# Kernel optimization log

Hardware: AMD Instinct MI355X
Metric: run time of the kernel (lower is better)

The kernel has to match this reference:

```python
import jax, jax.numpy as jnp
import numpy as np

N = 50000
E = 800000
IN_DIM = 128
HIDDEN = 32
HEADS = 4
OUT_DIM = 64
NEG_SLOPE = 0.2


def _glorot(key, shape):
    fan_in, fan_out = shape[0], shape[-1]
    lim = jnp.sqrt(6.0 / (fan_in + fan_out))
    return jax.random.uniform(key, shape, jnp.float32, -lim, lim)


def setup_inputs() -> dict:
    key = jax.random.key(0)
    ks = jax.random.split(key, 16)
    x = jax.random.normal(ks[0], (N, IN_DIM), jnp.float32)
    edge_index = jax.random.randint(ks[1], (2, E), 0, N, jnp.int64)
    # layer 0: in_dim -> hidden, heads, concat
    W1 = _glorot(ks[2], (IN_DIM, HEADS * HIDDEN))
    a_src1 = _glorot(ks[3], (HEADS, HIDDEN))
    a_dst1 = _glorot(ks[4], (HEADS, HIDDEN))
    b1 = jnp.zeros((HEADS * HIDDEN,), jnp.float32)
    # layer 1: hidden*heads -> hidden, heads, concat
    W2 = _glorot(ks[5], (HEADS * HIDDEN, HEADS * HIDDEN))
    a_src2 = _glorot(ks[6], (HEADS, HIDDEN))
    a_dst2 = _glorot(ks[7], (HEADS, HIDDEN))
    b2 = jnp.zeros((HEADS * HIDDEN,), jnp.float32)
    # layer 2: hidden*heads -> out_dim, heads, concat=False (mean over heads)
    W3 = _glorot(ks[8], (HEADS * HIDDEN, HEADS * OUT_DIM))
    a_src3 = _glorot(ks[9], (HEADS, OUT_DIM))
    a_dst3 = _glorot(ks[10], (HEADS, OUT_DIM))
    b3 = jnp.zeros((OUT_DIM,), jnp.float32)
    return {"x": x, "edge_index": edge_index,
            "W1": W1, "a_src1": a_src1, "a_dst1": a_dst1, "b1": b1,
            "W2": W2, "a_src2": a_src2, "a_dst2": a_dst2, "b2": b2,
            "W3": W3, "a_src3": a_src3, "a_dst3": a_dst3, "b3": b3}


def gat_conv(x, src, dst, W, a_src, a_dst, bias, out_ch, concat):
    # linear projection, per-head view: [N, H, C]
    h = (x @ W).reshape(N, HEADS, out_ch)
    # per-node attention logits, gathered to edges: [E, H]
    alpha_src = jnp.einsum('nhc,hc->nh', h, a_src)
    alpha_dst = jnp.einsum('nhc,hc->nh', h, a_dst)
    e = jax.nn.leaky_relu(alpha_src[src] + alpha_dst[dst], NEG_SLOPE)
    # segment softmax over incoming edges of each dst node
    m = jax.ops.segment_max(e, dst, num_segments=N)  # [N, H]
    m = jnp.where(jnp.isfinite(m), m, 0.0)
    p = jnp.exp(e - m[dst])  # [E, H]
    denom = jax.ops.segment_sum(p, dst, num_segments=N)  # [N, H]
    alpha = p / (denom[dst] + 1e-16)
    # weighted scatter-add of source features: [N, H, C]
    out = jax.ops.segment_sum(h[src] * alpha[:, :, None], dst, num_segments=N)
    if concat:
        return out.reshape(N, HEADS * out_ch) + bias
    return out.mean(axis=1) + bias


def reference(x, edge_index, W1, a_src1, a_dst1, b1, W2, a_src2, a_dst2, b2,
              W3, a_src3, a_dst3, b3):
    src, dst = edge_index[0], edge_index[1]
    x = gat_conv(x, src, dst, W1, a_src1, a_dst1, b1, HIDDEN, True)
    x = gat_conv(x, src, dst, W2, a_src2, a_dst2, b2, HIDDEN, True)
    x = gat_conv(x, src, dst, W3, a_src3, a_dst3, b3, OUT_DIM, False)
    return x
```

## Files before the change

kernel.cpp:

```cpp
#include <hip/hip_runtime.h>
#include <hip/hip_fp16.h>
#include <math.h>

#define NNODES 50000
#define NEDGES 800000

typedef _Float16 half8 __attribute__((ext_vector_type(8)));
typedef float floatx4 __attribute__((ext_vector_type(4)));


__global__ void zero_i32(int* __restrict__ p, int n) {
    int i = blockIdx.x * 256 + threadIdx.x;
    if (i < n) p[i] = 0;
}

__global__ void hist_kernel(const int* __restrict__ dst, int* __restrict__ counts, int e) {
    int i = blockIdx.x * 256 + threadIdx.x;
    if (i < e) atomicAdd(&counts[dst[i]], 1);
}

__global__ void scan1_kernel(const int* __restrict__ counts, int* __restrict__ row_ptr,
                             int* __restrict__ bsums, int n) {
    __shared__ int s[256];
    int tid = threadIdx.x;
    int i = blockIdx.x * 256 + tid;
    int v = (i < n) ? counts[i] : 0;
    s[tid] = v;
    __syncthreads();
    #pragma unroll
    for (int o = 1; o < 256; o <<= 1) {
        int t = (tid >= o) ? s[tid - o] : 0;
        __syncthreads();
        s[tid] += t;
        __syncthreads();
    }
    if (i < n) row_ptr[i + 1] = s[tid];
    if (tid == 255) bsums[blockIdx.x] = s[255];
}

__global__ void scan2_kernel(int* __restrict__ bsums, int nb) {
    __shared__ int s[256];
    int tid = threadIdx.x;
    int v = (tid < nb) ? bsums[tid] : 0;
    s[tid] = v;
    __syncthreads();
    #pragma unroll
    for (int o = 1; o < 256; o <<= 1) {
        int t = (tid >= o) ? s[tid - o] : 0;
        __syncthreads();
        s[tid] += t;
        __syncthreads();
    }
    if (tid < nb) bsums[tid] = s[tid] - v;
}

__global__ void scan3_kernel(int* __restrict__ row_ptr, const int* __restrict__ bsums,
                             int* __restrict__ cursor, int n) {
    int i = blockIdx.x * 256 + threadIdx.x;
    if (i < n) {
        row_ptr[i + 1] += bsums[blockIdx.x];
        cursor[i] = 0;
    }
    if (i == 0) row_ptr[0] = 0;
}

__global__ void fill_kernel(const int* __restrict__ src, const int* __restrict__ dst,
                            const int* __restrict__ row_ptr, int* __restrict__ cursor,
                            int* __restrict__ csr_src, int e) {
    int i = blockIdx.x * 256 + threadIdx.x;
    if (i < e) {
        int d = dst[i];
        int pos = atomicAdd(&cursor[d], 1);
        csr_src[row_ptr[d] + pos] = src[i];
    }
}

__global__ void prep_v_kernel(const float* __restrict__ W3, const float* __restrict__ as3,
                              const float* __restrict__ ad3, float* __restrict__ Vs,
                              float* __restrict__ Vd) {
    int id = blockIdx.x * 256 + threadIdx.x;
    if (id >= 1024) return;
    int which = id >> 9;
    int rem = id & 511;
    int k = rem >> 2;
    int hd = rem & 3;
    const float* av = which ? ad3 : as3;
    float s = 0.f;
    #pragma unroll 8
    for (int c = 0; c < 64; ++c)
        s += W3[(size_t)k * 256 + hd * 64 + c] * av[hd * 64 + c];
    (which ? Vd : Vs)[hd * 128 + k] = s;
}

__global__ void prep_wr_kernel(const float* __restrict__ W3, __half* __restrict__ Wr) {
    int id = blockIdx.x * 256 + threadIdx.x;
    if (id >= 64 * 512) return;
    int c = id >> 9;
    int rem = id & 511;
    int hd = rem >> 7;
    int k = rem & 127;
    Wr[(size_t)c * 512 + hd * 128 + k] = __float2half(W3[(size_t)k * 256 + hd * 64 + c]);
}


template <bool AF32, int LAYER>
__global__ __launch_bounds__(256, 3) void gemm_mfma(const void* __restrict__ A_,
                                                    const float* __restrict__ Wf,
                                                    const float* __restrict__ a_src,
                                                    const float* __restrict__ a_dst,
                                                    __half* __restrict__ H,
                                                    float* __restrict__ asrc,
                                                    float* __restrict__ adst, int n) {
    const int M = 128, CH = 32;
    __shared__ __half As[128][136];
    __shared__ __half Ws[64][136];
    int tid = threadIdx.x;
    int row0 = blockIdx.x * 128;
    int col0 = blockIdx.y * 64;

    if constexpr (AF32) {
        const float* Af = (const float*)A_;
        #pragma unroll
        for (int it = 0; it < 8; ++it) {
            int flat = tid + it * 256;
            int r = flat >> 4;
            int kq = (flat & 15) * 8;
            int gr = row0 + r;
            float4 v0 = {0.f, 0.f, 0.f, 0.f}, v1 = {0.f, 0.f, 0.f, 0.f};
            if (gr < n) {
                v0 = *(const float4*)&Af[(size_t)gr * 128 + kq];
                v1 = *(const float4*)&Af[(size_t)gr * 128 + kq + 4];
            }
            __half2 h0 = __floats2half2_rn(v0.x, v0.y);
            __half2 h1 = __floats2half2_rn(v0.z, v0.w);
            __half2 h2 = __floats2half2_rn(v1.x, v1.y);
            __half2 h3 = __floats2half2_rn(v1.z, v1.w);
            uint4 st = {*(unsigned*)&h0, *(unsigned*)&h1, *(unsigned*)&h2, *(unsigned*)&h3};
            *(uint4*)&As[r][kq] = st;
        }
    } else {
        const __half* Ah = (const __half*)A_;
        #pragma unroll
        for (int it = 0; it < 8; ++it) {
            int flat = tid + it * 256;
            int r = flat >> 4;
            int kq = (flat & 15) * 8;
            int gr = row0 + r;
            float4 v = {0.f, 0.f, 0.f, 0.f};
            if (gr < n) v = *(const float4*)&Ah[(size_t)gr * 128 + kq];
            *(float4*)&As[r][kq] = v;
        }
    }
    #pragma unroll
    for (int it = 0; it < 4; ++it) {
        int flat = tid + it * 256;
        int kp = flat >> 4;
        int c4 = (flat & 15) * 4;
        int k = kp * 2;
        float4 va = *(const float4*)&Wf[(size_t)k * M + col0 + c4];
        float4 vb = *(const float4*)&Wf[(size_t)(k + 1) * M + col0 + c4];
        *(__half2*)&Ws[c4 + 0][k] = __floats2half2_rn(va.x, vb.x);
        *(__half2*)&Ws[c4 + 1][k] = __floats2half2_rn(va.y, vb.y);
        *(__half2*)&Ws[c4 + 2][k] = __floats2half2_rn(va.z, vb.z);
        *(__half2*)&Ws[c4 + 3][k] = __floats2half2_rn(va.w, vb.w);
    }
    __syncthreads();

    int lane = tid & 63;
    int wid = tid >> 6;
    int wm = (wid >> 1) * 64;
    int wn = (wid & 1) * 32;
    int l15 = lane & 15;
    int l4 = lane >> 4;

    floatx4 acc[4][2];
    #pragma unroll
    for (int mf = 0; mf < 4; ++mf)
        #pragma unroll
        for (int nf = 0; nf < 2; ++nf) {
            floatx4 z = {0.f, 0.f, 0.f, 0.f};
            acc[mf][nf] = z;
        }

    #pragma unroll
    for (int ks = 0; ks < 4; ++ks) {
        int kb = ks * 32 + l4 * 8;
        half8 b0 = *(const half8*)&Ws[wn + l15][kb];
        half8 b1 = *(const half8*)&Ws[wn + 16 + l15][kb];
        #pragma unroll
        for (int mf = 0; mf < 4; ++mf) {
            half8 a = *(const half8*)&As[wm + mf * 16 + l15][kb];
            acc[mf][0] = __builtin_amdgcn_mfma_f32_16x16x32_f16(a, b0, acc[mf][0], 0, 0, 0);
            acc[mf][1] = __builtin_amdgcn_mfma_f32_16x16x32_f16(a, b1, acc[mf][1], 0, 0, 0);
        }
    }

    #pragma unroll
    for (int mf = 0; mf < 4; ++mf)
        #pragma unroll
        for (int r = 0; r < 4; ++r) {
            int gr = row0 + wm + mf * 16 + l4 * 4 + r;
            if (gr < n) {
                H[(size_t)gr * M + col0 + wn + l15] = __float2half(acc[mf][0][r]);
                H[(size_t)gr * M + col0 + wn + 16 + l15] = __float2half(acc[mf][1][r]);
            }
        }

    int hw = (col0 + wn) / CH;
    float vs0 = a_src[hw * CH + l15];
    float vs1 = a_src[hw * CH + 16 + l15];
    float vd0 = a_dst[hw * CH + l15];
    float vd1 = a_dst[hw * CH + 16 + l15];

    #pragma unroll
    for (int mf = 0; mf < 4; ++mf)
        #pragma unroll
        for (int r = 0; r < 4; ++r) {
            float ss = acc[mf][0][r] * vs0 + acc[mf][1][r] * vs1;
            float sd = acc[mf][0][r] * vd0 + acc[mf][1][r] * vd1;
            #pragma unroll
            for (int o = 1; o < 16; o <<= 1) {
                ss += __shfl_xor(ss, o);
                sd += __shfl_xor(sd, o);
            }
            int gr = row0 + wm + mf * 16 + l4 * 4 + r;
            if (l15 == 0 && gr < n) {
                asrc[(size_t)gr * 4 + hw] = ss;
                adst[(size_t)gr * 4 + hw] = sd;
            }
        }
}


template <int LAYER, bool FUSE_A3>
__global__ __launch_bounds__(256) void aggregate_kernel(
    const __half* __restrict__ h, const float* __restrict__ asrc,
    const float* __restrict__ adst, const int* __restrict__ csr_src,
    const int* __restrict__ row_ptr, const float* __restrict__ bias,
    const float* __restrict__ Vs, const float* __restrict__ Vd,
    __half* __restrict__ out, float* __restrict__ asrc3,
    float* __restrict__ adst3, int n) {
    __shared__ float lds[4][320];
    int wid = threadIdx.x >> 6;
    int lane = threadIdx.x & 63;
    int node = blockIdx.x * 4 + wid;
    if (node >= n) return;
    float* Wp4 = lds[wid];
    int* Ws = (int*)&lds[wid][256];
    int start = row_ptr[node];
    int end = row_ptr[node + 1];
    float4 ad = *(const float4*)&adst[(size_t)node * 4];
    int head = lane >> 4;

    float acc0 = 0.f, acc1 = 0.f, pw = 0.f;

    for (int base = start; base < end; base += 64) {
        int cnt = end - base;
        if (cnt > 64) cnt = 64;
        int s = 0;
        float4 pv = {0.f, 0.f, 0.f, 0.f};
        if (lane < cnt) {
            s = csr_src[base + lane];
            float4 a = *(const float4*)&asrc[(size_t)s * 4];
            float e0 = a.x + ad.x; e0 = (e0 > 0.f) ? e0 : 0.2f * e0;
            float e1 = a.y + ad.y; e1 = (e1 > 0.f) ? e1 : 0.2f * e1;
            float e2 = a.z + ad.z; e2 = (e2 > 0.f) ? e2 : 0.2f * e2;
            float e3 = a.w + ad.w; e3 = (e3 > 0.f) ? e3 : 0.2f * e3;
            pv.x = __expf(e0); pv.y = __expf(e1); pv.z = __expf(e2); pv.w = __expf(e3);
        }
        *(float4*)&Wp4[lane * 4] = pv;
        Ws[lane] = s;
        __builtin_amdgcn_wave_barrier();
        asm volatile("" ::: "memory");
        for (int jj = 0; jj < cnt; jj += 8) {
            float w[8]; int sa[8];
            #pragma unroll
            for (int u = 0; u < 8; ++u) {
                w[u] = Wp4[(jj + u) * 4 + head];
                sa[u] = Ws[jj + u];
            }
            unsigned raw[8];
            #pragma unroll
            for (int u = 0; u < 8; ++u)
                raw[u] = *(const unsigned*)(h + (size_t)sa[u] * 128 + lane * 2);
            #pragma unroll
            for (int u = 0; u < 8; ++u) {
                float2 f = __half22float2(*(const __half2*)&raw[u]);
                acc0 += w[u] * f.x;
                acc1 += w[u] * f.y;
                pw += w[u];
            }
        }
        __builtin_amdgcn_wave_barrier();
        asm volatile("" ::: "memory");
    }

    float inv = 1.f / (pw + 1e-16f);
    float2 b = *(const float2*)&bias[lane * 2];
    float o0 = acc0 * inv + b.x;
    float o1 = acc1 * inv + b.y;
    *(__half2*)&out[(size_t)node * 128 + lane * 2] = __floats2half2_rn(o0, o1);

    if constexpr (FUSE_A3) {
        float r[8];
        #pragma unroll
        for (int hd = 0; hd < 4; ++hd) {
            r[hd]     = o0 * Vs[hd * 128 + lane * 2] + o1 * Vs[hd * 128 + lane * 2 + 1];
            r[hd + 4] = o0 * Vd[hd * 128 + lane * 2] + o1 * Vd[hd * 128 + lane * 2 + 1];
        }
        #pragma unroll
        for (int o = 1; o < 64; o <<= 1) {
            #pragma unroll
            for (int q = 0; q < 8; ++q) r[q] += __shfl_xor(r[q], o);
        }
        if (lane == 0) {
            #pragma unroll
            for (int hd = 0; hd < 4; ++hd) {
                asrc3[(size_t)node * 4 + hd] = r[hd];
                adst3[(size_t)node * 4 + hd] = r[hd + 4];
            }
        }
    }
}


__global__ __launch_bounds__(256) void aggregate_x_kernel(
    const __half* __restrict__ A, const float* __restrict__ asrc,
    const float* __restrict__ adst, const int* __restrict__ csr_src,
    const int* __restrict__ row_ptr, __half* __restrict__ S, int n) {
    __shared__ float lds[4][320];
    int wid = threadIdx.x >> 6;
    int lane = threadIdx.x & 63;
    int node = blockIdx.x * 4 + wid;
    if (node >= n) return;
    float* Wp4 = lds[wid];
    int* Ws = (int*)&lds[wid][256];
    int start = row_ptr[node];
    int end = row_ptr[node + 1];
    float4 ad = *(const float4*)&adst[(size_t)node * 4];

    float a00 = 0.f, a01 = 0.f, a10 = 0.f, a11 = 0.f;
    float a20 = 0.f, a21 = 0.f, a30 = 0.f, a31 = 0.f;
    float4 psum = {0.f, 0.f, 0.f, 0.f};

    for (int base = start; base < end; base += 64) {
        int cnt = end - base;
        if (cnt > 64) cnt = 64;
        int s = 0;
        float4 pv = {0.f, 0.f, 0.f, 0.f};
        if (lane < cnt) {
            s = csr_src[base + lane];
            float4 a = *(const float4*)&asrc[(size_t)s * 4];
            float e0 = a.x + ad.x; e0 = (e0 > 0.f) ? e0 : 0.2f * e0;
            float e1 = a.y + ad.y; e1 = (e1 > 0.f) ? e1 : 0.2f * e1;
            float e2 = a.z + ad.z; e2 = (e2 > 0.f) ? e2 : 0.2f * e2;
            float e3 = a.w + ad.w; e3 = (e3 > 0.f) ? e3 : 0.2f * e3;
            pv.x = __expf(e0); pv.y = __expf(e1); pv.z = __expf(e2); pv.w = __expf(e3);
            psum.x += pv.x; psum.y += pv.y; psum.z += pv.z; psum.w += pv.w;
        }
        *(float4*)&Wp4[lane * 4] = pv;
        Ws[lane] = s;
        __builtin_amdgcn_wave_barrier();
        asm volatile("" ::: "memory");
        for (int jj = 0; jj < cnt; jj += 8) {
            int sa[8];
            #pragma unroll
            for (int u = 0; u < 8; ++u) sa[u] = Ws[jj + u];
            unsigned raw[8];
            #pragma unroll
            for (int u = 0; u < 8; ++u)
                raw[u] = *(const unsigned*)(A + (size_t)sa[u] * 128 + lane * 2);
            #pragma unroll
            for (int u = 0; u < 8; ++u) {
                float4 p = *(const float4*)&Wp4[(jj + u) * 4];
                float2 f = __half22float2(*(const __half2*)&raw[u]);
                a00 += p.x * f.x; a01 += p.x * f.y;
                a10 += p.y * f.x; a11 += p.y * f.y;
                a20 += p.z * f.x; a21 += p.z * f.y;
                a30 += p.w * f.x; a31 += p.w * f.y;
            }
        }
        __builtin_amdgcn_wave_barrier();
        asm volatile("" ::: "memory");
    }

    #pragma unroll
    for (int o = 1; o < 64; o <<= 1) {
        psum.x += __shfl_xor(psum.x, o);
        psum.y += __shfl_xor(psum.y, o);
        psum.z += __shfl_xor(psum.z, o);
        psum.w += __shfl_xor(psum.w, o);
    }
    float s0 = 0.25f / (psum.x + 1e-16f);
    float s1 = 0.25f / (psum.y + 1e-16f);
    float s2 = 0.25f / (psum.z + 1e-16f);
    float s3 = 0.25f / (psum.w + 1e-16f);
    size_t sb = (size_t)node * 512 + lane * 2;
    *(__half2*)&S[sb + 0 * 128] = __floats2half2_rn(a00 * s0, a01 * s0);
    *(__half2*)&S[sb + 1 * 128] = __floats2half2_rn(a10 * s1, a11 * s1);
    *(__half2*)&S[sb + 2 * 128] = __floats2half2_rn(a20 * s2, a21 * s2);
    *(__half2*)&S[sb + 3 * 128] = __floats2half2_rn(a30 * s3, a31 * s3);
}


__global__ __launch_bounds__(256, 3) void post_gemm(const __half* __restrict__ S,
                                                    const __half* __restrict__ Wr,
                                                    const float* __restrict__ b3,
                                                    float* __restrict__ out, int n) {
    __shared__ __half As[128][136];
    __shared__ __half Ws[64][136];
    int tid = threadIdx.x;
    int row0 = blockIdx.x * 128;
    int lane = tid & 63;
    int wid = tid >> 6;
    int wm = (wid >> 1) * 64;
    int wn = (wid & 1) * 32;
    int l15 = lane & 15;
    int l4 = lane >> 4;

    floatx4 acc[4][2];
    #pragma unroll
    for (int mf = 0; mf < 4; ++mf)
        #pragma unroll
        for (int nf = 0; nf < 2; ++nf) {
            floatx4 z = {0.f, 0.f, 0.f, 0.f};
            acc[mf][nf] = z;
        }

    for (int kb = 0; kb < 512; kb += 128) {
        #pragma unroll
        for (int it = 0; it < 8; ++it) {
            int flat = tid + it * 256;
            int r = flat >> 4;
            int kq = (flat & 15) * 8;
            int gr = row0 + r;
            float4 v = {0.f, 0.f, 0.f, 0.f};
            if (gr < n) v = *(const float4*)&S[(size_t)gr * 512 + kb + kq];
            *(float4*)&As[r][kq] = v;
        }
        #pragma unroll
        for (int it = 0; it < 4; ++it) {
            int flat = tid + it * 256;
            int r = flat >> 4;
            int kq = (flat & 15) * 8;
            *(float4*)&Ws[r][kq] = *(const float4*)&Wr[(size_t)r * 512 + kb + kq];
        }
        __syncthreads();
        #pragma unroll
        for (int ks = 0; ks < 4; ++ks) {
            int kk = ks * 32 + l4 * 8;
            half8 b0 = *(const half8*)&Ws[wn + l15][kk];
            half8 b1 = *(const half8*)&Ws[wn + 16 + l15][kk];
            #pragma unroll
            for (int mf = 0; mf < 4; ++mf) {
                half8 a = *(const half8*)&As[wm + mf * 16 + l15][kk];
                acc[mf][0] = __builtin_amdgcn_mfma_f32_16x16x32_f16(a, b0, acc[mf][0], 0, 0, 0);
                acc[mf][1] = __builtin_amdgcn_mfma_f32_16x16x32_f16(a, b1, acc[mf][1], 0, 0, 0);
            }
        }
        __syncthreads();
    }

    float bl = b3[wn + l15];
    float bh = b3[wn + 16 + l15];
    #pragma unroll
    for (int mf = 0; mf < 4; ++mf)
        #pragma unroll
        for (int r = 0; r < 4; ++r) {
            int gr = row0 + wm + mf * 16 + l4 * 4 + r;
            if (gr < n) {
                out[(size_t)gr * 64 + wn + l15] = acc[mf][0][r] + bl;
                out[(size_t)gr * 64 + wn + 16 + l15] = acc[mf][1][r] + bh;
            }
        }
}


extern "C" void kernel_launch(void* const* d_in, const int* in_sizes, int n_in,
                              void* d_out, int out_size, void* d_ws, size_t ws_size,
                              hipStream_t stream) {
    const float* x = (const float*)d_in[0];
    const int* ei = (const int*)d_in[1];
    const int* src = ei;
    const int* dst = ei + NEDGES;
    const float* W1 = (const float*)d_in[2];
    const float* as1 = (const float*)d_in[3];
    const float* ad1 = (const float*)d_in[4];
    const float* b1 = (const float*)d_in[5];
    const float* W2 = (const float*)d_in[6];
    const float* as2 = (const float*)d_in[7];
    const float* ad2 = (const float*)d_in[8];
    const float* b2 = (const float*)d_in[9];
    const float* W3 = (const float*)d_in[10];
    const float* as3 = (const float*)d_in[11];
    const float* ad3 = (const float*)d_in[12];
    const float* b3 = (const float*)d_in[13];

    char* ws = (char*)d_ws;
    size_t off = 0;
    auto take = [&](size_t bytes) -> char* {
        char* p = ws + off;
        off = (off + bytes + 255) & ~(size_t)255;
        return p;
    };
    int* csr = (int*)take((size_t)NEDGES * 4);
    int* row_ptr = (int*)take((size_t)(NNODES + 1) * 4);
    int* counts = (int*)take((size_t)NNODES * 4);
    int* cursor = (int*)take((size_t)NNODES * 4);
    int* bsums = (int*)take(1024 * 4);
    float* asrc = (float*)take((size_t)NNODES * 4 * 4);
    float* adst = (float*)take((size_t)NNODES * 4 * 4);
    float* asrc3 = (float*)take((size_t)NNODES * 4 * 4);
    float* adst3 = (float*)take((size_t)NNODES * 4 * 4);
    __half* hbuf = (__half*)take((size_t)NNODES * 128 * 2);
    __half* buf1h = (__half*)take((size_t)NNODES * 128 * 2);
    __half* Sbuf = (__half*)take((size_t)NNODES * 512 * 2);
    float* Vs = (float*)take(512 * 4);
    float* Vd = (float*)take(512 * 4);
    __half* Wr = (__half*)take((size_t)64 * 512 * 2);
    float* outp = (float*)d_out;

    int nbN = (NNODES + 255) / 256;
    int nbE = (NEDGES + 255) / 256;
    int gnodeAgg = (NNODES + 3) / 4;

    zero_i32<<<nbN, 256, 0, stream>>>(counts, NNODES);
    hist_kernel<<<nbE, 256, 0, stream>>>(dst, counts, NEDGES);
    scan1_kernel<<<nbN, 256, 0, stream>>>(counts, row_ptr, bsums, NNODES);
    scan2_kernel<<<1, 256, 0, stream>>>(bsums, nbN);
    scan3_kernel<<<nbN, 256, 0, stream>>>(row_ptr, bsums, cursor, NNODES);
    fill_kernel<<<nbE, 256, 0, stream>>>(src, dst, row_ptr, cursor, csr, NEDGES);
    prep_v_kernel<<<4, 256, 0, stream>>>(W3, as3, ad3, Vs, Vd);
    prep_wr_kernel<<<128, 256, 0, stream>>>(W3, Wr);

    dim3 gA((NNODES + 127) / 128, 2);

    gemm_mfma<true, 1><<<gA, 256, 0, stream>>>(x, W1, as1, ad1, hbuf, asrc, adst, NNODES);
    aggregate_kernel<1, false><<<gnodeAgg, 256, 0, stream>>>(
        hbuf, asrc, adst, csr, row_ptr, b1, nullptr, nullptr, buf1h, nullptr, nullptr, NNODES);

    gemm_mfma<false, 2><<<gA, 256, 0, stream>>>(buf1h, W2, as2, ad2, hbuf, asrc, adst, NNODES);
    aggregate_kernel<2, true><<<gnodeAgg, 256, 0, stream>>>(
        hbuf, asrc, adst, csr, row_ptr, b2, Vs, Vd, buf1h, asrc3, adst3, NNODES);

    aggregate_x_kernel<<<gnodeAgg, 256, 0, stream>>>(buf1h, asrc3, adst3, csr, row_ptr, Sbuf, NNODES);
    post_gemm<<<(NNODES + 127) / 128, 256, 0, stream>>>(Sbuf, Wr, b3, outp, NNODES);
}
```

Before: 281.6 us.

## Merge preprocessing kernels and fuse CSR fill into layer-1 GEMM launch

```diff
diff --git a/kernel.cpp b/kernel.cpp
--- a/kernel.cpp
+++ b/kernel.cpp
@@ -8,16 +8,6 @@
 typedef _Float16 half8 __attribute__((ext_vector_type(8)));
 typedef float floatx4 __attribute__((ext_vector_type(4)));
 
-
-__global__ void zero_i32(int* __restrict__ p, int n) {
-    int i = blockIdx.x * 256 + threadIdx.x;
-    if (i < n) p[i] = 0;
-}
-
-__global__ void hist_kernel(const int* __restrict__ dst, int* __restrict__ counts, int e) {
-    int i = blockIdx.x * 256 + threadIdx.x;
-    if (i < e) atomicAdd(&counts[dst[i]], 1);
-}
 
 __global__ void scan1_kernel(const int* __restrict__ counts, int* __restrict__ row_ptr,
                              int* __restrict__ bsums, int n) {
@@ -64,59 +54,51 @@
     if (i == 0) row_ptr[0] = 0;
 }
 
-__global__ void fill_kernel(const int* __restrict__ src, const int* __restrict__ dst,
-                            const int* __restrict__ row_ptr, int* __restrict__ cursor,
-                            int* __restrict__ csr_src, int e) {
-    int i = blockIdx.x * 256 + threadIdx.x;
-    if (i < e) {
-        int d = dst[i];
-        int pos = atomicAdd(&cursor[d], 1);
-        csr_src[row_ptr[d] + pos] = src[i];
-    }
-}
-
-__global__ void prep_v_kernel(const float* __restrict__ W3, const float* __restrict__ as3,
-                              const float* __restrict__ ad3, float* __restrict__ Vs,
-                              float* __restrict__ Vd) {
-    int id = blockIdx.x * 256 + threadIdx.x;
-    if (id >= 1024) return;
-    int which = id >> 9;
-    int rem = id & 511;
-    int k = rem >> 2;
-    int hd = rem & 3;
-    const float* av = which ? ad3 : as3;
-    float s = 0.f;
-    #pragma unroll 8
-    for (int c = 0; c < 64; ++c)
-        s += W3[(size_t)k * 256 + hd * 64 + c] * av[hd * 64 + c];
-    (which ? Vd : Vs)[hd * 128 + k] = s;
-}
-
-__global__ void prep_wr_kernel(const float* __restrict__ W3, __half* __restrict__ Wr) {
-    int id = blockIdx.x * 256 + threadIdx.x;
-    if (id >= 64 * 512) return;
-    int c = id >> 9;
-    int rem = id & 511;
-    int hd = rem >> 7;
-    int k = rem & 127;
-    Wr[(size_t)c * 512 + hd * 128 + k] = __float2half(W3[(size_t)k * 256 + hd * 64 + c]);
-}
-
-
-template <bool AF32, int LAYER>
-__global__ __launch_bounds__(256, 3) void gemm_mfma(const void* __restrict__ A_,
-                                                    const float* __restrict__ Wf,
-                                                    const float* __restrict__ a_src,
-                                                    const float* __restrict__ a_dst,
-                                                    __half* __restrict__ H,
-                                                    float* __restrict__ asrc,
-                                                    float* __restrict__ adst, int n) {
+
+__global__ void hist_prep_kernel(const int* __restrict__ dst, int* __restrict__ counts,
+                                 const float* __restrict__ W3, const float* __restrict__ as3,
+                                 const float* __restrict__ ad3, float* __restrict__ Vs,
+                                 float* __restrict__ Vd, __half* __restrict__ Wr) {
+    int b = blockIdx.x;
+    int tid = threadIdx.x;
+    if (b < 3125) {
+        int i = b * 256 + tid;
+        if (i < NEDGES) atomicAdd(&counts[dst[i]], 1);
+    } else if (b < 3129) {
+        int id = (b - 3125) * 256 + tid;
+        int which = id >> 9;
+        int rem = id & 511;
+        int k = rem >> 2;
+        int hd = rem & 3;
+        const float* av = which ? ad3 : as3;
+        float s = 0.f;
+        #pragma unroll 8
+        for (int c = 0; c < 64; ++c)
+            s += W3[(size_t)k * 256 + hd * 64 + c] * av[hd * 64 + c];
+        (which ? Vd : Vs)[hd * 128 + k] = s;
+    } else {
+        int id = (b - 3129) * 256 + tid;
+        int c = id >> 9;
+        int rem = id & 511;
+        int hd = rem >> 7;
+        int k = rem & 127;
+        Wr[(size_t)c * 512 + hd * 128 + k] = __float2half(W3[(size_t)k * 256 + hd * 64 + c]);
+    }
+}
+
+
+template <bool AF32>
+__device__ __forceinline__ void gemm_body(__half (*As)[136], __half (*Ws)[136], int bid,
+                                          const void* __restrict__ A_,
+                                          const float* __restrict__ Wf,
+                                          const float* __restrict__ a_src,
+                                          const float* __restrict__ a_dst,
+                                          __half* __restrict__ H,
+                                          float* __restrict__ asrc,
+                                          float* __restrict__ adst, int n, int tid) {
     const int M = 128, CH = 32;
-    __shared__ __half As[128][136];
-    __shared__ __half Ws[64][136];
-    int tid = threadIdx.x;
-    int row0 = blockIdx.x * 128;
-    int col0 = blockIdx.y * 64;
+    int row0 = (bid >> 1) * 128;
+    int col0 = (bid & 1) * 64;
 
     if constexpr (AF32) {
         const float* Af = (const float*)A_;
@@ -229,6 +211,42 @@
                 adst[(size_t)gr * 4 + hw] = sd;
             }
         }
+}
+
+
+__global__ __launch_bounds__(256, 3) void fill_gemm1(
+    const float* __restrict__ x, const float* __restrict__ W1,
+    const float* __restrict__ as1, const float* __restrict__ ad1,
+    __half* __restrict__ H, float* __restrict__ asrc, float* __restrict__ adst,
+    const int* __restrict__ src, const int* __restrict__ dst,
+    const int* __restrict__ row_ptr, int* __restrict__ cursor,
+    int* __restrict__ csr_src, int n) {
+    __shared__ __half As[128][136];
+    __shared__ __half Ws[64][136];
+    int tid = threadIdx.x;
+    if (blockIdx.x < 782) {
+        gemm_body<true>(As, Ws, blockIdx.x, x, W1, as1, ad1, H, asrc, adst, n, tid);
+    } else {
+        int i = (blockIdx.x - 782) * 256 + tid;
+        if (i < NEDGES) {
+            int d = dst[i];
+            int pos = atomicAdd(&cursor[d], 1);
+            csr_src[row_ptr[d] + pos] = src[i];
+        }
+    }
+}
+
+
+__global__ __launch_bounds__(256, 3) void gemm_mfma2(const __half* __restrict__ A,
+                                                     const float* __restrict__ Wf,
+                                                     const float* __restrict__ a_src,
+                                                     const float* __restrict__ a_dst,
+                                                     __half* __restrict__ H,
+                                                     float* __restrict__ asrc,
+                                                     float* __restrict__ adst, int n) {
+    __shared__ __half As[128][136];
+    __shared__ __half Ws[64][136];
+    gemm_body<false>(As, Ws, blockIdx.x, A, Wf, a_src, a_dst, H, asrc, adst, n, threadIdx.x);
 }
 
 
@@ -521,25 +539,20 @@
     float* outp = (float*)d_out;
 
     int nbN = (NNODES + 255) / 256;
-    int nbE = (NEDGES + 255) / 256;
     int gnodeAgg = (NNODES + 3) / 4;
 
-    zero_i32<<<nbN, 256, 0, stream>>>(counts, NNODES);
-    hist_kernel<<<nbE, 256, 0, stream>>>(dst, counts, NEDGES);
+    hipMemsetAsync(counts, 0, (size_t)NNODES * 4, stream);
+    hist_prep_kernel<<<3257, 256, 0, stream>>>(dst, counts, W3, as3, ad3, Vs, Vd, Wr);
     scan1_kernel<<<nbN, 256, 0, stream>>>(counts, row_ptr, bsums, NNODES);
     scan2_kernel<<<1, 256, 0, stream>>>(bsums, nbN);
     scan3_kernel<<<nbN, 256, 0, stream>>>(row_ptr, bsums, cursor, NNODES);
-    fill_kernel<<<nbE, 256, 0, stream>>>(src, dst, row_ptr, cursor, csr, NEDGES);
-    prep_v_kernel<<<4, 256, 0, stream>>>(W3, as3, ad3, Vs, Vd);
-    prep_wr_kernel<<<128, 256, 0, stream>>>(W3, Wr);
-
-    dim3 gA((NNODES + 127) / 128, 2);
-
-    gemm_mfma<true, 1><<<gA, 256, 0, stream>>>(x, W1, as1, ad1, hbuf, asrc, adst, NNODES);
+
+    fill_gemm1<<<3907, 256, 0, stream>>>(x, W1, as1, ad1, hbuf, asrc, adst,
+                                         src, dst, row_ptr, cursor, csr, NNODES);
     aggregate_kernel<1, false><<<gnodeAgg, 256, 0, stream>>>(
         hbuf, asrc, adst, csr, row_ptr, b1, nullptr, nullptr, buf1h, nullptr, nullptr, NNODES);
 
-    gemm_mfma<false, 2><<<gA, 256, 0, stream>>>(buf1h, W2, as2, ad2, hbuf, asrc, adst, NNODES);
+    gemm_mfma2<<<782, 256, 0, stream>>>(buf1h, W2, as2, ad2, hbuf, asrc, adst, NNODES);
     aggregate_kernel<2, true><<<gnodeAgg, 256, 0, stream>>>(
         hbuf, asrc, adst, csr, row_ptr, b2, Vs, Vd, buf1h, asrc3, adst3, NNODES);
 
```

New measurement: 268.7 us. 4.6% less time.
